# Kernel optimization log

Hardware: AMD Instinct MI355X
Metric: run time of the kernel (lower is better)

The kernel has to match this reference:

```python
import jax, jax.numpy as jnp
import numpy as np

H = 128; N = 64; B = 128; L = 3; F = 7; E = 64; LAT = 128
NEG = -1e9

def _ln(x, g, b, eps=1e-5):
    m = jnp.mean(x, axis=-1, keepdims=True)
    v = jnp.mean((x - m) ** 2, axis=-1, keepdims=True)
    return (x - m) / jnp.sqrt(v + eps) * g + b

def setup_inputs() -> dict:
    key = jax.random.key(0)
    ks = iter(jax.random.split(key, 64))
    def w(shape, s=0.05):
        return (jax.random.normal(next(ks), shape, dtype=jnp.float32) * s)
    inp = {}
    inp['battery_features'] = jax.random.normal(next(ks), (B, F), dtype=jnp.float32)
    inp['material_embeddings'] = jax.random.normal(next(ks), (B, N, E), dtype=jnp.float32)
    inp['node_mask'] = (jax.random.uniform(next(ks), (B, N)) > 0.2).astype(jnp.float32)
    # material encoder: Linear(E,H), LN, ReLU, Linear(H,H), LN, ReLU
    inp['enc_W1'] = w((E, H)); inp['enc_b1'] = jnp.zeros((H,))
    inp['enc_g1'] = jnp.ones((H,)); inp['enc_B1'] = jnp.zeros((H,))
    inp['enc_W2'] = w((H, H)); inp['enc_b2'] = jnp.zeros((H,))
    inp['enc_g2'] = jnp.ones((H,)); inp['enc_B2'] = jnp.zeros((H,))
    # per-layer GATv2 params (stacked over L layers)
    inp['Wq'] = w((L, H, H)); inp['bq'] = jnp.zeros((L, H))
    inp['Wk'] = w((L, H, H)); inp['bk'] = jnp.zeros((L, H))
    inp['Wv'] = w((L, H, H)); inp['bv'] = jnp.zeros((L, H))
    inp['We1'] = w((L, 2 * H, H)); inp['be1'] = jnp.zeros((L, H))
    inp['We2'] = w((L, H)); inp['be2'] = jnp.zeros((L,))
    inp['Wo'] = w((L, H, H)); inp['bo'] = jnp.zeros((L, H))
    inp['o_g'] = jnp.ones((L, H)); inp['o_B'] = jnp.zeros((L, H))
    # legacy decoder: Linear(F+H,H), LN, ReLU, Linear(H,LAT), LN, ReLU, Linear(LAT,F)
    inp['dW1'] = w((F + H, H)); inp['db1'] = jnp.zeros((H,))
    inp['dg1'] = jnp.ones((H,)); inp['dB1'] = jnp.zeros((H,))
    inp['dW2'] = w((H, LAT)); inp['db2'] = jnp.zeros((LAT,))
    inp['dg2'] = jnp.ones((LAT,)); inp['dB2'] = jnp.zeros((LAT,))
    inp['dW3'] = w((LAT, F)); inp['db3'] = jnp.zeros((F,))
    return inp

def reference(battery_features, material_embeddings, node_mask,
              enc_W1, enc_b1, enc_g1, enc_B1, enc_W2, enc_b2, enc_g2, enc_B2,
              Wq, bq, Wk, bk, Wv, bv, We1, be1, We2, be2, Wo, bo, o_g, o_B,
              dW1, db1, dg1, dB1, dW2, db2, dg2, dB2, dW3, db3):
    # material encoder (dropout=0 / eval)
    x = material_embeddings  # [B,N,E]
    h = jax.nn.relu(_ln(x @ enc_W1 + enc_b1, enc_g1, enc_B1))
    h = jax.nn.relu(_ln(h @ enc_W2 + enc_b2, enc_g2, enc_B2))
    x = h * node_mask[..., None]  # [B,N,H]
    mask2d = node_mask[:, :, None] * node_mask[:, None, :]  # [B,N,N]
    nlayers = Wq.shape[0]
    for l in range(nlayers):
        q = x @ Wq[l] + bq[l]
        k = x @ Wk[l] + bk[l]
        v = x @ Wv[l] + bv[l]
        # edge MLP on concat(q_i, k_j): split first linear, avoid concat materialization
        hq = q @ We1[l, :H]          # [B,N,H]
        hk = k @ We1[l, H:]          # [B,N,H]
        eh = jax.nn.relu(hq[:, :, None, :] + hk[:, None, :, :] + be1[l])  # [B,N,N,H]
        scores = jnp.einsum('bijh,h->bij', eh, We2[l]) + be2[l]
        scores = jnp.where(mask2d > 0, scores, NEG)
        attn = jax.nn.softmax(scores, axis=-1) * mask2d
        agg = jnp.einsum('bij,bjh->bih', attn, v)
        x = jax.nn.relu(_ln(agg @ Wo[l] + bo[l], o_g[l], o_B[l]))
        x = x * node_mask[..., None]
    # masked mean pooling
    denom = jnp.clip(jnp.sum(node_mask, axis=1, keepdims=True), 1.0, None)
    pooled = jnp.sum(x * node_mask[..., None], axis=1) / denom  # [B,H]
    d = jnp.concatenate([battery_features, pooled], axis=-1)
    z = jax.nn.relu(_ln(d @ dW1 + db1, dg1, dB1))
    z = jax.nn.relu(_ln(z @ dW2 + db2, dg2, dB2))
    return z @ dW3 + db3  # [B,F] predicted properties
```

## Files before the change

### kernel.cpp

```cpp
#include <hip/hip_runtime.h>


constexpr float EPS = 1e-5f;
constexpr float NEGI = -1e9f;

typedef __bf16 bf16x8 __attribute__((ext_vector_type(8)));
typedef float floatx4 __attribute__((ext_vector_type(4)));
typedef _Float16 h2 __attribute__((ext_vector_type(2)));
union U32H2 { unsigned int u; h2 h; };

__device__ __forceinline__ unsigned int pkh2(float a, float b) {
  U32H2 u; u.h[0] = (_Float16)a; u.h[1] = (_Float16)b; return u.u;
}
__device__ __forceinline__ float fdot2h(h2 a, h2 b, float c) {
#if __has_builtin(__builtin_amdgcn_fdot2)
  return __builtin_amdgcn_fdot2(a, b, c, false);
#else
  return c + (float)a[0] * (float)b[0] + (float)a[1] * (float)b[1];
#endif
}
__device__ __forceinline__ bf16x8 cvt8(const float* p) {
  float t[8];
  *(float4*)t = *(const float4*)p;
  *(float4*)(t + 4) = *(const float4*)(p + 4);
  bf16x8 r;
#pragma unroll
  for (int j = 0; j < 8; ++j) r[j] = (__bf16)t[j];
  return r;
}

__global__ __launch_bounds__(256) void prep_kernel(
    const float* __restrict__ Wq, const float* __restrict__ bq,
    const float* __restrict__ Wk, const float* __restrict__ bk,
    const float* __restrict__ bv, const float* __restrict__ We1,
    const float* __restrict__ be1,
    const float* __restrict__ eW1, const float* __restrict__ eW2,
    const float* __restrict__ Wv, const float* __restrict__ Wo,
    __bf16* __restrict__ w1pk, __bf16* __restrict__ w2pk,
    __bf16* __restrict__ wcatpk, __bf16* __restrict__ wopk,
    float* __restrict__ bcat) {
  int tid = threadIdx.x, blk = blockIdx.x;
  if (blk < 48) {
    __shared__ float sB[128 * 16];
    __shared__ float sF[128 * 17];
    int jb = blk >> 3, cc = blk & 7;
    int l = jb >> 1, w = jb & 1;
    const float* A = (w ? Wk : Wq) + l * 16384;
    const float* Bm = We1 + l * 32768 + w * 16384;
    int c0 = cc * 16;
    for (int idx = tid; idx < 2048; idx += 256) {
      int m = idx >> 4, c = idx & 15;
      sB[idx] = Bm[m * 128 + c0 + c];
    }
    __syncthreads();
    int r = tid >> 1, c8 = (tid & 1) * 8;
    float acc[8] = {};
    const float4* A4 = (const float4*)(A + r * 128);
#pragma unroll 8
    for (int k4 = 0; k4 < 32; ++k4) {
      float4 a = A4[k4];
      float av[4] = {a.x, a.y, a.z, a.w};
#pragma unroll
      for (int kk = 0; kk < 4; ++kk)
#pragma unroll
        for (int c = 0; c < 8; ++c)
          acc[c] = fmaf(av[kk], sB[(k4 * 4 + kk) * 16 + c8 + c], acc[c]);
    }
    for (int c = 0; c < 8; ++c) sF[r * 17 + c8 + c] = acc[c];
    __syncthreads();
    int kc = tid >> 6, ln = tid & 63;
    int k0 = kc * 32 + (ln >> 4) * 8, n = ln & 15;
    bf16x8 pk;
#pragma unroll
    for (int j = 0; j < 8; ++j) pk[j] = (__bf16)sF[(k0 + j) * 17 + n];
    int ntg = 8 + w * 8 + cc;
    *((bf16x8*)(wcatpk + l * 49152) + (ntg * 4 + kc) * 64 + ln) = pk;
  } else if (blk < 56) {
    int job = blk - 48;
    const float* src;
    __bf16* dst;
    int KCH = 4;
    if (job == 0) { src = eW1; dst = w1pk; KCH = 2; }
    else if (job == 1) { src = eW2; dst = w2pk; }
    else if (job < 5) { int l = job - 2; src = Wv + l * 16384; dst = wcatpk + l * 49152; }
    else { int l = job - 5; src = Wo + l * 16384; dst = wopk + l * 16384; }
    for (int s = tid; s < 8 * KCH * 64; s += 256) {
      int ln = s & 63, q = s >> 6;
      int kc = q % KCH, nt = q / KCH;
      int k0 = kc * 32 + (ln >> 4) * 8, n = nt * 16 + (ln & 15);
      bf16x8 pk;
#pragma unroll
      for (int j = 0; j < 8; ++j) pk[j] = (__bf16)src[(k0 + j) * 128 + n];
      *((bf16x8*)dst + (nt * KCH + kc) * 64 + ln) = pk;
    }
  } else {
    for (int idx = tid; idx < 3 * 384; idx += 256) {
      int l = idx / 384, c = idx % 384;
      float val;
      if (c < 128) {
        val = bv[l * 128 + c];
      } else if (c < 256) {
        int cc2 = c - 128;
        float s = 0.f;
        for (int k = 0; k < 128; ++k) s += bq[l * 128 + k] * We1[l * 32768 + k * 128 + cc2];
        val = s;
      } else {
        int cc2 = c - 256;
        float s = be1[l * 128 + cc2];
        for (int k = 0; k < 128; ++k) s += bk[l * 128 + k] * We1[l * 32768 + 16384 + k * 128 + cc2];
        val = s;
      }
      bcat[l * 384 + c] = val;
    }
  }
}

__device__ __forceinline__ void ln16(float* sT, __bf16* SX, const float* __restrict__ g,
                                     const float* __restrict__ be, float mreg,
                                     int i0, int tid, int mode) {
  int r = tid >> 4, c0 = tid & 15;
  const float* base = sT + r * 132;
  float s = 0.f, q = 0.f;
#pragma unroll
  for (int k = 0; k < 8; ++k) { float v = base[c0 + k * 16]; s += v; q += v * v; }
  s += __shfl_xor(s, 1); s += __shfl_xor(s, 2); s += __shfl_xor(s, 4); s += __shfl_xor(s, 8);
  q += __shfl_xor(q, 1); q += __shfl_xor(q, 2); q += __shfl_xor(q, 4); q += __shfl_xor(q, 8);
  float m = s * (1.f / 128.f);
  float rs = rsqrtf(fmaxf(q * (1.f / 128.f) - m * m, 0.f) + EPS);
  float mk = (mode >= 1) ? __shfl(mreg, i0 + r) : 1.f;
  int c8 = c0 * 8;
  float vals[8];
  *(float4*)vals = *(const float4*)(base + c8);
  *(float4*)(vals + 4) = *(const float4*)(base + c8 + 4);
#pragma unroll
  for (int k = 0; k < 8; ++k)
    vals[k] = fmaxf((vals[k] - m) * rs * g[c8 + k] + be[c8 + k], 0.f) * mk;
  if (mode < 2) {
    bf16x8 pk;
#pragma unroll
    for (int k = 0; k < 8; ++k) pk[k] = (__bf16)vals[k];
    ((bf16x8*)SX)[(c8 >> 5) * 64 + ((c8 >> 3) & 3) * 16 + r] = pk;
  } else {
    *(float4*)(sT + r * 132 + c8) = *(float4*)vals;
    *(float4*)(sT + r * 132 + c8 + 4) = *(float4*)(vals + 4);
  }
}

__device__ __forceinline__ void qkv_tail(
    const __bf16* SX, float* sTv, float* sTq, float* sTk,
    int b, int i0, const __bf16* __restrict__ wc, const float* __restrict__ bc,
    unsigned int* __restrict__ hqg_o, unsigned int* __restrict__ hkT_o,
    __bf16* __restrict__ vpk_o, int tid) {
  int lane = tid & 63, wv = tid >> 6, quad = lane >> 4, cl = lane & 15;
  bf16x8 ax[4];
#pragma unroll
  for (int kc = 0; kc < 4; ++kc) ax[kc] = ((const bf16x8*)SX)[kc * 64 + lane];
  floatx4 acc[6];
#pragma unroll
  for (int n = 0; n < 6; ++n) acc[n] = 0;
#pragma unroll
  for (int kc = 0; kc < 4; ++kc)
#pragma unroll
    for (int n = 0; n < 6; ++n) {
      bf16x8 bw = ((const bf16x8*)wc)[((wv + n * 4) * 4 + kc) * 64 + lane];
      acc[n] = __builtin_amdgcn_mfma_f32_16x16x32_bf16(ax[kc], bw, acc[n], 0, 0, 0);
    }
#pragma unroll
  for (int n = 0; n < 6; ++n) {
    int nt = wv + n * 4;
    float* dstT;
    int coll;
    float bb;
    if (nt < 8) { dstT = sTv; coll = nt * 16 + cl; bb = bc[coll]; }
    else if (nt < 16) { dstT = sTq; coll = (nt - 8) * 16 + cl; bb = bc[128 + coll]; }
    else { dstT = sTk; coll = (nt - 16) * 16 + cl; bb = bc[256 + coll]; }
#pragma unroll
    for (int r = 0; r < 4; ++r) dstT[(quad * 4 + r) * 132 + coll] = acc[n][r] + bb;
  }
  __syncthreads();
  {
    int nt = tid >> 5, dq = (tid >> 4) & 1, c2 = tid & 15;
    int kcv = i0 >> 5, qg = ((i0 & 31) >> 3) + dq;
    bf16x8 pk;
#pragma unroll
    for (int jj = 0; jj < 8; ++jj) pk[jj] = (__bf16)sTv[(dq * 8 + jj) * 132 + nt * 16 + c2];
    ((bf16x8*)vpk_o)[b * 1024 + (nt * 2 + kcv) * 64 + qg * 16 + c2] = pk;
  }
  {
    int r = tid >> 4, c0 = tid & 15;
    float vq[8];
    *(float4*)vq = *(const float4*)(sTq + r * 132 + c0 * 8);
    *(float4*)(vq + 4) = *(const float4*)(sTq + r * 132 + c0 * 8 + 4);
    uint4 oq;
    oq.x = pkh2(vq[0], vq[1]); oq.y = pkh2(vq[2], vq[3]);
    oq.z = pkh2(vq[4], vq[5]); oq.w = pkh2(vq[6], vq[7]);
    *(uint4*)(hqg_o + (b * 64 + i0 + r) * 64 + c0 * 4) = oq;
  }
  {
    int jr = tid & 15, hpg = tid >> 4;
    float vk[8];
    *(float4*)vk = *(const float4*)(sTk + jr * 132 + hpg * 8);
    *(float4*)(vk + 4) = *(const float4*)(sTk + jr * 132 + hpg * 8 + 4);
    int jg = i0 + jr;
#pragma unroll
    for (int t = 0; t < 4; ++t)
      hkT_o[b * 4096 + (hpg * 4 + t) * 64 + jg] = pkh2(vk[2 * t], vk[2 * t + 1]);
  }
}

__global__ __launch_bounds__(256) void enc_qkv_kernel(
    const float* __restrict__ emb, const float* __restrict__ mask,
    const float* __restrict__ eb1, const float* __restrict__ eg1, const float* __restrict__ eB1,
    const float* __restrict__ eb2, const float* __restrict__ eg2, const float* __restrict__ eB2,
    const __bf16* __restrict__ w1pk, const __bf16* __restrict__ w2pk,
    const __bf16* __restrict__ wcat0, const float* __restrict__ bcat0,
    unsigned int* __restrict__ hqg, unsigned int* __restrict__ hkT,
    __bf16* __restrict__ vpk) {
  __shared__ __align__(16) float sT[16 * 132];
  __shared__ __align__(16) __bf16 SX[2048];
  __shared__ __align__(16) float sTv[16 * 132], sTq[16 * 132], sTk[16 * 132];
  int tid = threadIdx.x, blk = blockIdx.x;
  int lane = tid & 63, wv = tid >> 6, quad = lane >> 4, cl = lane & 15;
  int b = blk >> 2, i0 = (blk & 3) * 16;
  float mreg = mask[b * 64 + lane];

  {
    bf16x8 a1[2];
#pragma unroll
    for (int kc = 0; kc < 2; ++kc)
      a1[kc] = cvt8(emb + (b * 64 + i0 + cl) * 64 + kc * 32 + quad * 8);
    floatx4 acc[2];
    acc[0] = 0; acc[1] = 0;
#pragma unroll
    for (int kc = 0; kc < 2; ++kc)
#pragma unroll
      for (int n = 0; n < 2; ++n) {
        bf16x8 bw = ((const bf16x8*)w1pk)[((wv + n * 4) * 2 + kc) * 64 + lane];
        acc[n] = __builtin_amdgcn_mfma_f32_16x16x32_bf16(a1[kc], bw, acc[n], 0, 0, 0);
      }
#pragma unroll
    for (int n = 0; n < 2; ++n) {
      int col = (wv + n * 4) * 16 + cl;
      float bb = eb1[col];
#pragma unroll
      for (int r = 0; r < 4; ++r) sT[(quad * 4 + r) * 132 + col] = acc[n][r] + bb;
    }
  }
  __syncthreads();
  ln16(sT, SX, eg1, eB1, mreg, i0, tid, 0);
  __syncthreads();
  {
    bf16x8 a2[4];
#pragma unroll
    for (int kc = 0; kc < 4; ++kc) a2[kc] = ((const bf16x8*)SX)[kc * 64 + lane];
    floatx4 acc[2];
    acc[0] = 0; acc[1] = 0;
#pragma unroll
    for (int kc = 0; kc < 4; ++kc)
#pragma unroll
      for (int n = 0; n < 2; ++n) {
        bf16x8 bw = ((const bf16x8*)w2pk)[((wv + n * 4) * 4 + kc) * 64 + lane];
        acc[n] = __builtin_amdgcn_mfma_f32_16x16x32_bf16(a2[kc], bw, acc[n], 0, 0, 0);
      }
#pragma unroll
    for (int n = 0; n < 2; ++n) {
      int col = (wv + n * 4) * 16 + cl;
      float bb = eb2[col];
#pragma unroll
      for (int r = 0; r < 4; ++r) sT[(quad * 4 + r) * 132 + col] = acc[n][r] + bb;
    }
  }
  __syncthreads();
  ln16(sT, SX, eg2, eB2, mreg, i0, tid, 1);
  __syncthreads();
  qkv_tail(SX, sTv, sTq, sTk, b, i0, wcat0, bcat0, hqg, hkT, vpk, tid);
}

template <bool LAST>
__global__ __launch_bounds__(256) void layer_kernel(
    const unsigned int* __restrict__ hq_in, const unsigned int* __restrict__ hkT_in,
    const __bf16* __restrict__ vp_in, const float* __restrict__ mask,
    const float* __restrict__ We2l, const float* __restrict__ be2p,
    const __bf16* __restrict__ wopk_l, const float* __restrict__ bo_l,
    const float* __restrict__ og_l, const float* __restrict__ oB_l,
    const __bf16* __restrict__ wcat_n, const float* __restrict__ bcat_n,
    unsigned int* __restrict__ hq_out, unsigned int* __restrict__ hkT_out,
    __bf16* __restrict__ vpk_out, float* __restrict__ poolp) {
  __shared__ __align__(16) unsigned int sHK[64 * 64];
  __shared__ __align__(16) unsigned int hqS[16 * 64];
  __shared__ unsigned int w2h[64];
  __shared__ __align__(16) __bf16 pA[16 * 64];
  __shared__ __align__(16) __bf16 pA2[2048];
  __shared__ __align__(16) __bf16 SX[2048];
  __shared__ __align__(16) float sT[16 * 132];
  __shared__ __align__(16) float sTv[16 * 132], sTq[16 * 132], sTk[16 * 132];
  int tid = threadIdx.x, blk = blockIdx.x;
  int lane = tid & 63, wv = tid >> 6, quad = lane >> 4, cl = lane & 15;
  int b = blk >> 2, i0 = (blk & 3) * 16;
  float mreg = mask[b * 64 + lane];

  {
    const uint4* src = (const uint4*)(hkT_in + b * 4096);
    uint4* dst = (uint4*)sHK;
#pragma unroll
    for (int it = 0; it < 4; ++it) dst[it * 256 + tid] = src[it * 256 + tid];
    ((uint4*)hqS)[tid] = ((const uint4*)(hq_in + (b * 64 + i0) * 64))[tid];
    if (tid < 64) w2h[tid] = pkh2(We2l[2 * tid], We2l[2 * tid + 1]);
  }
  __syncthreads();

  {
    int j = lane;
    float accs[4] = {0.f, 0.f, 0.f, 0.f};
    h2 hz = {(_Float16)0.0f, (_Float16)0.0f};
#pragma unroll 4
    for (int c4 = 0; c4 < 16; ++c4) {
      uint4 w2v = *(const uint4*)(w2h + c4 * 4);
      int hp0 = c4 * 4;
      uint4 hkv;
      hkv.x = sHK[(hp0 + 0) * 64 + j];
      hkv.y = sHK[(hp0 + 1) * 64 + j];
      hkv.z = sHK[(hp0 + 2) * 64 + j];
      hkv.w = sHK[(hp0 + 3) * 64 + j];
#pragma unroll
      for (int il = 0; il < 4; ++il) {
        uint4 hqv = *(const uint4*)(hqS + (wv * 4 + il) * 64 + hp0);
        U32H2 ha, hb, wc2;
        h2 s2;
        ha.u = hqv.x; hb.u = hkv.x; wc2.u = w2v.x;
        s2 = __builtin_elementwise_max(ha.h + hb.h, hz);
        accs[il] = fdot2h(s2, wc2.h, accs[il]);
        ha.u = hqv.y; hb.u = hkv.y; wc2.u = w2v.y;
        s2 = __builtin_elementwise_max(ha.h + hb.h, hz);
        accs[il] = fdot2h(s2, wc2.h, accs[il]);
        ha.u = hqv.z; hb.u = hkv.z; wc2.u = w2v.z;
        s2 = __builtin_elementwise_max(ha.h + hb.h, hz);
        accs[il] = fdot2h(s2, wc2.h, accs[il]);
        ha.u = hqv.w; hb.u = hkv.w; wc2.u = w2v.w;
        s2 = __builtin_elementwise_max(ha.h + hb.h, hz);
        accs[il] = fdot2h(s2, wc2.h, accs[il]);
      }
    }
    float be2v = be2p[0];
    float mj = mreg;
#pragma unroll
    for (int kk = 0; kk < 4; ++kk) {
      int il = wv * 4 + kk;
      float mi = __shfl(mreg, i0 + il);
      float m2 = mi * mj;
      float sc = (m2 > 0.f) ? accs[kk] + be2v : NEGI;
      float mx = sc;
#pragma unroll
      for (int off = 32; off >= 1; off >>= 1) mx = fmaxf(mx, __shfl_xor(mx, off));
      float p = __expf(sc - mx);
      float sm = p;
#pragma unroll
      for (int off = 32; off >= 1; off >>= 1) sm += __shfl_xor(sm, off);
      float a = p / sm * m2;
      pA[((j >> 5) * 64 + ((j >> 3) & 3) * 16 + il) * 8 + (j & 7)] = (__bf16)a;
    }
  }
  __syncthreads();

  {
    bf16x8 aat[2];
#pragma unroll
    for (int kc = 0; kc < 2; ++kc) aat[kc] = ((const bf16x8*)pA)[kc * 64 + lane];
    floatx4 acc[2];
    acc[0] = 0; acc[1] = 0;
#pragma unroll
    for (int kc = 0; kc < 2; ++kc)
#pragma unroll
      for (int n = 0; n < 2; ++n) {
        bf16x8 bw = ((const bf16x8*)vp_in)[b * 1024 + ((wv + n * 4) * 2 + kc) * 64 + lane];
        acc[n] = __builtin_amdgcn_mfma_f32_16x16x32_bf16(aat[kc], bw, acc[n], 0, 0, 0);
      }
#pragma unroll
    for (int n = 0; n < 2; ++n) {
      int hcol = (wv + n * 4) * 16 + cl;
#pragma unroll
      for (int r = 0; r < 4; ++r) {
        int i = quad * 4 + r;
        pA2[((hcol >> 5) * 64 + ((hcol >> 3) & 3) * 16 + i) * 8 + (hcol & 7)] =
            (__bf16)acc[n][r];
      }
    }
  }
  __syncthreads();

  {
    bf16x8 ag[4];
#pragma unroll
    for (int kc = 0; kc < 4; ++kc) ag[kc] = ((const bf16x8*)pA2)[kc * 64 + lane];
    floatx4 acc[2];
    acc[0] = 0; acc[1] = 0;
#pragma unroll
    for (int kc = 0; kc < 4; ++kc)
#pragma unroll
      for (int n = 0; n < 2; ++n) {
        bf16x8 bw = ((const bf16x8*)wopk_l)[((wv + n * 4) * 4 + kc) * 64 + lane];
        acc[n] = __builtin_amdgcn_mfma_f32_16x16x32_bf16(ag[kc], bw, acc[n], 0, 0, 0);
      }
#pragma unroll
    for (int n = 0; n < 2; ++n) {
      int col = (wv + n * 4) * 16 + cl;
      float bb = bo_l[col];
#pragma unroll
      for (int r = 0; r < 4; ++r) sT[(quad * 4 + r) * 132 + col] = acc[n][r] + bb;
    }
  }
  __syncthreads();
  ln16(sT, SX, og_l, oB_l, mreg, i0, tid, LAST ? 2 : 1);
  __syncthreads();
  if (!LAST) {
    qkv_tail(SX, sTv, sTq, sTk, b, i0, wcat_n, bcat_n, hq_out, hkT_out, vpk_out, tid);
  } else {
    if (tid < 128) {
      float s = 0.f;
#pragma unroll
      for (int r = 0; r < 16; ++r) s += sT[r * 132 + tid];
      poolp[blk * 128 + tid] = s;
    }
  }
}

__device__ __forceinline__ float ln128(float val, float g, float be, int t, float* red) {
  float s = val, q = val * val;
#pragma unroll
  for (int off = 32; off >= 1; off >>= 1) {
    s += __shfl_xor(s, off);
    q += __shfl_xor(q, off);
  }
  if ((t & 63) == 0) { red[(t >> 6) * 2] = s; red[(t >> 6) * 2 + 1] = q; }
  __syncthreads();
  float S = red[0] + red[2], Q = red[1] + red[3];
  __syncthreads();
  float m = S * (1.f / 128.f);
  float var = Q * (1.f / 128.f) - m * m;
  float r = rsqrtf(fmaxf(var, 0.f) + EPS);
  return (val - m) * r * g + be;
}

__global__ __launch_bounds__(128) void dec_kernel(
    const float* __restrict__ bfeat, const float* __restrict__ poolp,
    const float* __restrict__ mask,
    const float* __restrict__ dW1, const float* __restrict__ db1,
    const float* __restrict__ dg1, const float* __restrict__ dB1,
    const float* __restrict__ dW2, const float* __restrict__ db2,
    const float* __restrict__ dg2, const float* __restrict__ dB2,
    const float* __restrict__ dW3, const float* __restrict__ db3,
    float* __restrict__ out) {
  __shared__ float sd[136];
  __shared__ float sz[128];
  __shared__ float red[4];
  __shared__ float s_mk[64];
  int b = blockIdx.x, t = threadIdx.x;
  if (t < 64) s_mk[t] = mask[b * 64 + t];
  __syncthreads();
  float den = 0.f;
#pragma unroll
  for (int i = 0; i < 64; ++i) den += s_mk[i];
  den = fmaxf(den, 1.f);
  float pooled = poolp[(b * 4 + 0) * 128 + t] + poolp[(b * 4 + 1) * 128 + t] +
                 poolp[(b * 4 + 2) * 128 + t] + poolp[(b * 4 + 3) * 128 + t];
  if (t < 7) sd[t] = bfeat[b * 7 + t];
  sd[7 + t] = pooled / den;
  __syncthreads();

  float z = db1[t];
  for (int k = 0; k < 135; ++k) z = fmaf(sd[k], dW1[k * 128 + t], z);
  z = ln128(z, dg1[t], dB1[t], t, red);
  z = fmaxf(z, 0.f);
  sz[t] = z;
  __syncthreads();

  float z2 = db2[t];
  for (int k = 0; k < 128; ++k) z2 = fmaf(sz[k], dW2[k * 128 + t], z2);
  z2 = ln128(z2, dg2[t], dB2[t], t, red);
  z2 = fmaxf(z2, 0.f);
  sz[t] = z2;
  __syncthreads();

  if (t < 7) {
    float o = db3[t];
    for (int k = 0; k < 128; ++k) o = fmaf(sz[k], dW3[k * 7 + t], o);
    out[b * 7 + t] = o;
  }
}

extern "C" void kernel_launch(void* const* d_in, const int* in_sizes, int n_in,
                              void* d_out, int out_size, void* d_ws, size_t ws_size,
                              hipStream_t stream) {
  const float* bf   = (const float*)d_in[0];
  const float* emb  = (const float*)d_in[1];
  const float* mask = (const float*)d_in[2];
  const float* eW1 = (const float*)d_in[3];
  const float* eb1 = (const float*)d_in[4];
  const float* eg1 = (const float*)d_in[5];
  const float* eB1 = (const float*)d_in[6];
  const float* eW2 = (const float*)d_in[7];
  const float* eb2 = (const float*)d_in[8];
  const float* eg2 = (const float*)d_in[9];
  const float* eB2 = (const float*)d_in[10];
  const float* Wq = (const float*)d_in[11];
  const float* bq = (const float*)d_in[12];
  const float* Wk = (const float*)d_in[13];
  const float* bk = (const float*)d_in[14];
  const float* Wv = (const float*)d_in[15];
  const float* bv = (const float*)d_in[16];
  const float* We1 = (const float*)d_in[17];
  const float* be1 = (const float*)d_in[18];
  const float* We2 = (const float*)d_in[19];
  const float* be2 = (const float*)d_in[20];
  const float* Wo = (const float*)d_in[21];
  const float* bo = (const float*)d_in[22];
  const float* og = (const float*)d_in[23];
  const float* oB = (const float*)d_in[24];
  const float* dW1 = (const float*)d_in[25];
  const float* db1 = (const float*)d_in[26];
  const float* dg1 = (const float*)d_in[27];
  const float* dB1 = (const float*)d_in[28];
  const float* dW2 = (const float*)d_in[29];
  const float* db2 = (const float*)d_in[30];
  const float* dg2 = (const float*)d_in[31];
  const float* dB2 = (const float*)d_in[32];
  const float* dW3 = (const float*)d_in[33];
  const float* db3 = (const float*)d_in[34];
  float* out = (float*)d_out;

  char* ws = (char*)d_ws;
  float* bcat = (float*)ws;
  __bf16* w1pk   = (__bf16*)(ws + 8192);
  __bf16* w2pk   = (__bf16*)(ws + 24576);
  __bf16* wcatpk = (__bf16*)(ws + 57344);
  __bf16* wopk   = (__bf16*)(ws + 352256);
  unsigned int* hqg = (unsigned int*)(ws + 524288);
  unsigned int* hkT = (unsigned int*)(ws + 4718592);
  __bf16* vpk = (__bf16*)(ws + 8912896);
  float* poolp = (float*)(ws + 13107200);

  prep_kernel<<<57, 256, 0, stream>>>(Wq, bq, Wk, bk, bv, We1, be1,
                                      eW1, eW2, Wv, Wo, w1pk, w2pk, wcatpk, wopk, bcat);
  enc_qkv_kernel<<<512, 256, 0, stream>>>(emb, mask, eb1, eg1, eB1, eb2, eg2, eB2,
                                          w1pk, w2pk, wcatpk, bcat, hqg, hkT, vpk);
  layer_kernel<false><<<512, 256, 0, stream>>>(
      hqg, hkT, vpk, mask, We2, be2, wopk, bo, og, oB,
      wcatpk + 49152, bcat + 384,
      hqg + 524288, hkT + 524288, vpk + 1048576, nullptr);
  layer_kernel<false><<<512, 256, 0, stream>>>(
      hqg + 524288, hkT + 524288, vpk + 1048576, mask, We2 + 128, be2 + 1,
      wopk + 16384, bo + 128, og + 128, oB + 128,
      wcatpk + 2 * 49152, bcat + 2 * 384,
      hqg, hkT, vpk, nullptr);
  layer_kernel<true><<<512, 256, 0, stream>>>(
      hqg, hkT, vpk, mask, We2 + 256, be2 + 2,
      wopk + 2 * 16384, bo + 256, og + 256, oB + 256,
      nullptr, nullptr, nullptr, nullptr, nullptr, poolp);
  dec_kernel<<<128, 128, 0, stream>>>(bf, poolp, mask, dW1, db1, dg1, dB1,
                                      dW2, db2, dg2, dB2, dW3, db3, out);
}
```

Measured before the change: 204.5 us.

## Fuse decoder into last layer via atomic counter, cut LDS for occupancy

The separate decoder kernel is removed. The last block of each batch, found with an atomic per-batch counter, runs the decoder MLP inside the final layer kernel, so one launch and its gap go away. The key tensor is now read straight from global memory instead of being staged in LDS. Shared buffers are aliased into one byte array and launch bounds request 4 blocks per SM, to raise occupancy. The cost is uncached global reads in the score loop, an added memset, and cross-block synchronization through atomics.

```diff
diff --git a/kernel.cpp b/kernel.cpp
--- a/kernel.cpp
+++ b/kernel.cpp
@@ -216,9 +216,9 @@
     const __bf16* __restrict__ wcat0, const float* __restrict__ bcat0,
     unsigned int* __restrict__ hqg, unsigned int* __restrict__ hkT,
     __bf16* __restrict__ vpk) {
-  __shared__ __align__(16) float sT[16 * 132];
   __shared__ __align__(16) __bf16 SX[2048];
   __shared__ __align__(16) float sTv[16 * 132], sTq[16 * 132], sTk[16 * 132];
+  float* sT = sTv;
   int tid = threadIdx.x, blk = blockIdx.x;
   int lane = tid & 63, wv = tid >> 6, quad = lane >> 4, cl = lane & 15;
   int b = blk >> 2, i0 = (blk & 3) * 16;
@@ -277,7 +277,7 @@
 }
 
 template <bool LAST>
-__global__ __launch_bounds__(256) void layer_kernel(
+__global__ __launch_bounds__(256, 4) void layer_kernel(
     const unsigned int* __restrict__ hq_in, const unsigned int* __restrict__ hkT_in,
     const __bf16* __restrict__ vp_in, const float* __restrict__ mask,
     const float* __restrict__ We2l, const float* __restrict__ be2p,
@@ -285,25 +285,31 @@
     const float* __restrict__ og_l, const float* __restrict__ oB_l,
     const __bf16* __restrict__ wcat_n, const float* __restrict__ bcat_n,
     unsigned int* __restrict__ hq_out, unsigned int* __restrict__ hkT_out,
-    __bf16* __restrict__ vpk_out, float* __restrict__ poolp) {
-  __shared__ __align__(16) unsigned int sHK[64 * 64];
-  __shared__ __align__(16) unsigned int hqS[16 * 64];
-  __shared__ unsigned int w2h[64];
-  __shared__ __align__(16) __bf16 pA[16 * 64];
-  __shared__ __align__(16) __bf16 pA2[2048];
-  __shared__ __align__(16) __bf16 SX[2048];
-  __shared__ __align__(16) float sT[16 * 132];
-  __shared__ __align__(16) float sTv[16 * 132], sTq[16 * 132], sTk[16 * 132];
+    __bf16* __restrict__ vpk_out, float* __restrict__ poolp,
+    unsigned int* __restrict__ bctr, const float* __restrict__ bfeat,
+    const float* __restrict__ dW1, const float* __restrict__ db1,
+    const float* __restrict__ dg1, const float* __restrict__ dB1,
+    const float* __restrict__ dW2, const float* __restrict__ db2,
+    const float* __restrict__ dg2, const float* __restrict__ dB2,
+    const float* __restrict__ dW3, const float* __restrict__ db3,
+    float* __restrict__ out) {
+  __shared__ __align__(16) char SM[40960];
+  unsigned int* hqS = (unsigned int*)(SM + 0);
+  unsigned int* w2h = (unsigned int*)(SM + 4096);
+  __bf16* pA  = (__bf16*)(SM + 4352);
+  __bf16* pA2 = (__bf16*)(SM + 6400);
+  __bf16* SX  = (__bf16*)(SM + 10496);
+  float* sT   = (float*)(SM + 14592);
+  float* sTv  = sT;
+  float* sTq  = (float*)(SM + 23040);
+  float* sTk  = (float*)(SM + 31488);
+  unsigned int* flg = (unsigned int*)(SM + 39936);
   int tid = threadIdx.x, blk = blockIdx.x;
   int lane = tid & 63, wv = tid >> 6, quad = lane >> 4, cl = lane & 15;
   int b = blk >> 2, i0 = (blk & 3) * 16;
   float mreg = mask[b * 64 + lane];
 
   {
-    const uint4* src = (const uint4*)(hkT_in + b * 4096);
-    uint4* dst = (uint4*)sHK;
-#pragma unroll
-    for (int it = 0; it < 4; ++it) dst[it * 256 + tid] = src[it * 256 + tid];
     ((uint4*)hqS)[tid] = ((const uint4*)(hq_in + (b * 64 + i0) * 64))[tid];
     if (tid < 64) w2h[tid] = pkh2(We2l[2 * tid], We2l[2 * tid + 1]);
   }
@@ -311,6 +317,7 @@
 
   {
     int j = lane;
+    const unsigned int* hkg = hkT_in + b * 4096;
     float accs[4] = {0.f, 0.f, 0.f, 0.f};
     h2 hz = {(_Float16)0.0f, (_Float16)0.0f};
 #pragma unroll 4
@@ -318,10 +325,10 @@
       uint4 w2v = *(const uint4*)(w2h + c4 * 4);
       int hp0 = c4 * 4;
       uint4 hkv;
-      hkv.x = sHK[(hp0 + 0) * 64 + j];
-      hkv.y = sHK[(hp0 + 1) * 64 + j];
-      hkv.z = sHK[(hp0 + 2) * 64 + j];
-      hkv.w = sHK[(hp0 + 3) * 64 + j];
+      hkv.x = hkg[(hp0 + 0) * 64 + j];
+      hkv.y = hkg[(hp0 + 1) * 64 + j];
+      hkv.z = hkg[(hp0 + 2) * 64 + j];
+      hkv.w = hkg[(hp0 + 3) * 64 + j];
 #pragma unroll
       for (int il = 0; il < 4; ++il) {
         uint4 hqv = *(const uint4*)(hqS + (wv * 4 + il) * 64 + hp0);
@@ -421,70 +428,80 @@
       for (int r = 0; r < 16; ++r) s += sT[r * 132 + tid];
       poolp[blk * 128 + tid] = s;
     }
-  }
-}
-
-__device__ __forceinline__ float ln128(float val, float g, float be, int t, float* red) {
-  float s = val, q = val * val;
-#pragma unroll
-  for (int off = 32; off >= 1; off >>= 1) {
-    s += __shfl_xor(s, off);
-    q += __shfl_xor(q, off);
-  }
-  if ((t & 63) == 0) { red[(t >> 6) * 2] = s; red[(t >> 6) * 2 + 1] = q; }
-  __syncthreads();
-  float S = red[0] + red[2], Q = red[1] + red[3];
-  __syncthreads();
-  float m = S * (1.f / 128.f);
-  float var = Q * (1.f / 128.f) - m * m;
-  float r = rsqrtf(fmaxf(var, 0.f) + EPS);
-  return (val - m) * r * g + be;
-}
-
-__global__ __launch_bounds__(128) void dec_kernel(
-    const float* __restrict__ bfeat, const float* __restrict__ poolp,
-    const float* __restrict__ mask,
-    const float* __restrict__ dW1, const float* __restrict__ db1,
-    const float* __restrict__ dg1, const float* __restrict__ dB1,
-    const float* __restrict__ dW2, const float* __restrict__ db2,
-    const float* __restrict__ dg2, const float* __restrict__ dB2,
-    const float* __restrict__ dW3, const float* __restrict__ db3,
-    float* __restrict__ out) {
-  __shared__ float sd[136];
-  __shared__ float sz[128];
-  __shared__ float red[4];
-  __shared__ float s_mk[64];
-  int b = blockIdx.x, t = threadIdx.x;
-  if (t < 64) s_mk[t] = mask[b * 64 + t];
-  __syncthreads();
-  float den = 0.f;
-#pragma unroll
-  for (int i = 0; i < 64; ++i) den += s_mk[i];
-  den = fmaxf(den, 1.f);
-  float pooled = poolp[(b * 4 + 0) * 128 + t] + poolp[(b * 4 + 1) * 128 + t] +
-                 poolp[(b * 4 + 2) * 128 + t] + poolp[(b * 4 + 3) * 128 + t];
-  if (t < 7) sd[t] = bfeat[b * 7 + t];
-  sd[7 + t] = pooled / den;
-  __syncthreads();
-
-  float z = db1[t];
-  for (int k = 0; k < 135; ++k) z = fmaf(sd[k], dW1[k * 128 + t], z);
-  z = ln128(z, dg1[t], dB1[t], t, red);
-  z = fmaxf(z, 0.f);
-  sz[t] = z;
-  __syncthreads();
-
-  float z2 = db2[t];
-  for (int k = 0; k < 128; ++k) z2 = fmaf(sz[k], dW2[k * 128 + t], z2);
-  z2 = ln128(z2, dg2[t], dB2[t], t, red);
-  z2 = fmaxf(z2, 0.f);
-  sz[t] = z2;
-  __syncthreads();
-
-  if (t < 7) {
-    float o = db3[t];
-    for (int k = 0; k < 128; ++k) o = fmaf(sz[k], dW3[k * 7 + t], o);
-    out[b * 7 + t] = o;
+    __syncthreads();
+    if (tid == 0) {
+      __threadfence();
+      unsigned int old = __hip_atomic_fetch_add(bctr + b, 1u, __ATOMIC_ACQ_REL,
+                                                __HIP_MEMORY_SCOPE_AGENT);
+      *flg = old;
+    }
+    __syncthreads();
+    if (*flg != 3u) return;
+    __threadfence();
+
+    float* sd   = (float*)(SM + 0);
+    float* red  = (float*)(SM + 4096);
+    float* part = (float*)(SM + 6400);
+    float* szz  = (float*)(SM + 10496);
+    float den = mreg;
+#pragma unroll
+    for (int off = 32; off >= 1; off >>= 1) den += __shfl_xor(den, off);
+    den = fmaxf(den, 1.f);
+    if (tid < 7) sd[tid] = bfeat[b * 7 + tid];
+    if (tid < 128) {
+      float pooled = poolp[(b * 4 + 0) * 128 + tid] + poolp[(b * 4 + 1) * 128 + tid] +
+                     poolp[(b * 4 + 2) * 128 + tid] + poolp[(b * 4 + 3) * 128 + tid];
+      sd[7 + tid] = pooled / den;
+    }
+    __syncthreads();
+    int t = tid & 127, g2 = tid >> 7;
+    {
+      float zp = 0.f;
+      for (int k = g2; k < 135; k += 2) zp = fmaf(sd[k], dW1[k * 128 + t], zp);
+      part[g2 * 128 + t] = zp;
+    }
+    __syncthreads();
+    {
+      float z = db1[t] + part[t] + part[128 + t];
+      float s = z, q = z * z;
+#pragma unroll
+      for (int off = 32; off >= 1; off >>= 1) { s += __shfl_xor(s, off); q += __shfl_xor(q, off); }
+      if (tid < 128 && lane == 0) { red[(tid >> 6) * 2] = s; red[(tid >> 6) * 2 + 1] = q; }
+      __syncthreads();
+      float S = red[0] + red[2], Q = red[1] + red[3];
+      float m = S * (1.f / 128.f);
+      float rs = rsqrtf(fmaxf(Q * (1.f / 128.f) - m * m, 0.f) + EPS);
+      z = fmaxf((z - m) * rs * dg1[t] + dB1[t], 0.f);
+      __syncthreads();
+      if (tid < 128) szz[t] = z;
+    }
+    __syncthreads();
+    {
+      float zp = 0.f;
+      for (int k = g2; k < 128; k += 2) zp = fmaf(szz[k], dW2[k * 128 + t], zp);
+      part[g2 * 128 + t] = zp;
+    }
+    __syncthreads();
+    {
+      float y = db2[t] + part[t] + part[128 + t];
+      float s = y, q = y * y;
+#pragma unroll
+      for (int off = 32; off >= 1; off >>= 1) { s += __shfl_xor(s, off); q += __shfl_xor(q, off); }
+      if (tid < 128 && lane == 0) { red[(tid >> 6) * 2] = s; red[(tid >> 6) * 2 + 1] = q; }
+      __syncthreads();
+      float S = red[0] + red[2], Q = red[1] + red[3];
+      float m = S * (1.f / 128.f);
+      float rs = rsqrtf(fmaxf(Q * (1.f / 128.f) - m * m, 0.f) + EPS);
+      y = fmaxf((y - m) * rs * dg2[t] + dB2[t], 0.f);
+      __syncthreads();
+      if (tid < 128) szz[t] = y;
+    }
+    __syncthreads();
+    if (tid < 7) {
+      float o = db3[tid];
+      for (int k = 0; k < 128; ++k) o = fmaf(szz[k], dW3[k * 7 + tid], o);
+      out[b * 7 + tid] = o;
+    }
   }
 }
 
@@ -529,7 +546,8 @@
   float* out = (float*)d_out;
 
   char* ws = (char*)d_ws;
-  float* bcat = (float*)ws;
+  unsigned int* bctr = (unsigned int*)ws;
+  float* bcat = (float*)(ws + 1024);
   __bf16* w1pk   = (__bf16*)(ws + 8192);
   __bf16* w2pk   = (__bf16*)(ws + 24576);
   __bf16* wcatpk = (__bf16*)(ws + 57344);
@@ -539,6 +557,8 @@
   __bf16* vpk = (__bf16*)(ws + 8912896);
   float* poolp = (float*)(ws + 13107200);
 
+  hipMemsetAsync(d_ws, 0, 512, stream);
+
   prep_kernel<<<57, 256, 0, stream>>>(Wq, bq, Wk, bk, bv, We1, be1,
                                       eW1, eW2, Wv, Wo, w1pk, w2pk, wcatpk, wopk, bcat);
   enc_qkv_kernel<<<512, 256, 0, stream>>>(emb, mask, eb1, eg1, eB1, eb2, eg2, eB2,
@@ -546,16 +566,19 @@
   layer_kernel<false><<<512, 256, 0, stream>>>(
       hqg, hkT, vpk, mask, We2, be2, wopk, bo, og, oB,
       wcatpk + 49152, bcat + 384,
-      hqg + 524288, hkT + 524288, vpk + 1048576, nullptr);
+      hqg + 524288, hkT + 524288, vpk + 1048576, nullptr,
+      nullptr, nullptr, nullptr, nullptr, nullptr, nullptr,
+      nullptr, nullptr, nullptr, nullptr, nullptr, nullptr, nullptr);
   layer_kernel<false><<<512, 256, 0, stream>>>(
       hqg + 524288, hkT + 524288, vpk + 1048576, mask, We2 + 128, be2 + 1,
       wopk + 16384, bo + 128, og + 128, oB + 128,
       wcatpk + 2 * 49152, bcat + 2 * 384,
-      hqg, hkT, vpk, nullptr);
+      hqg, hkT, vpk, nullptr,
+      nullptr, nullptr, nullptr, nullptr, nullptr, nullptr,
+      nullptr, nullptr, nullptr, nullptr, nullptr, nullptr, nullptr);
   layer_kernel<true><<<512, 256, 0, stream>>>(
       hqg, hkT, vpk, mask, We2 + 256, be2 + 2,
       wopk + 2 * 16384, bo + 256, og + 256, oB + 256,
-      nullptr, nullptr, nullptr, nullptr, nullptr, poolp);
-  dec_kernel<<<128, 128, 0, stream>>>(bf, poolp, mask, dW1, db1, dg1, dB1,
-                                      dW2, db2, dg2, dB2, dW3, db3, out);
-}
+      nullptr, nullptr, nullptr, nullptr, nullptr, poolp,
+      bctr, bf, dW1, db1, dg1, dB1, dW2, db2, dg2, dB2, dW3, db3, out);
+}
```

New measurement: 254.6 us. 24.5% more time.

## Cut LDS footprint in layer kernel to raise occupancy, read hk from global

Applied to the files above, without the earlier changes.

The layer kernel no longer stages the per-batch transposed hk tile (16 KB) in LDS. Each wave now loads it directly from global memory, relying on L1/L2 to serve the four blocks that share a batch. The remaining shared buffers are packed into one 40 KB array with sT aliased onto sTv, and launch_bounds now asks for 4 blocks per CU. The encoder kernel also aliases sT onto sTv. The trade is higher occupancy against global-memory latency in the hot score loop. The bcat workspace offset also moves.

```diff
diff --git a/kernel.cpp b/kernel.cpp
--- a/kernel.cpp
+++ b/kernel.cpp
@@ -216,9 +216,9 @@
     const __bf16* __restrict__ wcat0, const float* __restrict__ bcat0,
     unsigned int* __restrict__ hqg, unsigned int* __restrict__ hkT,
     __bf16* __restrict__ vpk) {
-  __shared__ __align__(16) float sT[16 * 132];
   __shared__ __align__(16) __bf16 SX[2048];
   __shared__ __align__(16) float sTv[16 * 132], sTq[16 * 132], sTk[16 * 132];
+  float* sT = sTv;
   int tid = threadIdx.x, blk = blockIdx.x;
   int lane = tid & 63, wv = tid >> 6, quad = lane >> 4, cl = lane & 15;
   int b = blk >> 2, i0 = (blk & 3) * 16;
@@ -277,7 +277,7 @@
 }
 
 template <bool LAST>
-__global__ __launch_bounds__(256) void layer_kernel(
+__global__ __launch_bounds__(256, 4) void layer_kernel(
     const unsigned int* __restrict__ hq_in, const unsigned int* __restrict__ hkT_in,
     const __bf16* __restrict__ vp_in, const float* __restrict__ mask,
     const float* __restrict__ We2l, const float* __restrict__ be2p,
@@ -286,24 +286,22 @@
     const __bf16* __restrict__ wcat_n, const float* __restrict__ bcat_n,
     unsigned int* __restrict__ hq_out, unsigned int* __restrict__ hkT_out,
     __bf16* __restrict__ vpk_out, float* __restrict__ poolp) {
-  __shared__ __align__(16) unsigned int sHK[64 * 64];
-  __shared__ __align__(16) unsigned int hqS[16 * 64];
-  __shared__ unsigned int w2h[64];
-  __shared__ __align__(16) __bf16 pA[16 * 64];
-  __shared__ __align__(16) __bf16 pA2[2048];
-  __shared__ __align__(16) __bf16 SX[2048];
-  __shared__ __align__(16) float sT[16 * 132];
-  __shared__ __align__(16) float sTv[16 * 132], sTq[16 * 132], sTk[16 * 132];
+  __shared__ __align__(16) char SM[40960];
+  unsigned int* hqS = (unsigned int*)(SM + 0);
+  unsigned int* w2h = (unsigned int*)(SM + 4096);
+  __bf16* pA  = (__bf16*)(SM + 4352);
+  __bf16* pA2 = (__bf16*)(SM + 6400);
+  __bf16* SX  = (__bf16*)(SM + 10496);
+  float* sT   = (float*)(SM + 14592);
+  float* sTv  = sT;
+  float* sTq  = (float*)(SM + 23040);
+  float* sTk  = (float*)(SM + 31488);
   int tid = threadIdx.x, blk = blockIdx.x;
   int lane = tid & 63, wv = tid >> 6, quad = lane >> 4, cl = lane & 15;
   int b = blk >> 2, i0 = (blk & 3) * 16;
   float mreg = mask[b * 64 + lane];
 
   {
-    const uint4* src = (const uint4*)(hkT_in + b * 4096);
-    uint4* dst = (uint4*)sHK;
-#pragma unroll
-    for (int it = 0; it < 4; ++it) dst[it * 256 + tid] = src[it * 256 + tid];
     ((uint4*)hqS)[tid] = ((const uint4*)(hq_in + (b * 64 + i0) * 64))[tid];
     if (tid < 64) w2h[tid] = pkh2(We2l[2 * tid], We2l[2 * tid + 1]);
   }
@@ -311,6 +309,7 @@
 
   {
     int j = lane;
+    const unsigned int* hkg = hkT_in + b * 4096;
     float accs[4] = {0.f, 0.f, 0.f, 0.f};
     h2 hz = {(_Float16)0.0f, (_Float16)0.0f};
 #pragma unroll 4
@@ -318,10 +317,10 @@
       uint4 w2v = *(const uint4*)(w2h + c4 * 4);
       int hp0 = c4 * 4;
       uint4 hkv;
-      hkv.x = sHK[(hp0 + 0) * 64 + j];
-      hkv.y = sHK[(hp0 + 1) * 64 + j];
-      hkv.z = sHK[(hp0 + 2) * 64 + j];
-      hkv.w = sHK[(hp0 + 3) * 64 + j];
+      hkv.x = hkg[(hp0 + 0) * 64 + j];
+      hkv.y = hkg[(hp0 + 1) * 64 + j];
+      hkv.z = hkg[(hp0 + 2) * 64 + j];
+      hkv.w = hkg[(hp0 + 3) * 64 + j];
 #pragma unroll
       for (int il = 0; il < 4; ++il) {
         uint4 hqv = *(const uint4*)(hqS + (wv * 4 + il) * 64 + hp0);
@@ -529,7 +528,7 @@
   float* out = (float*)d_out;
 
   char* ws = (char*)d_ws;
-  float* bcat = (float*)ws;
+  float* bcat = (float*)(ws + 1024);
   __bf16* w1pk   = (__bf16*)(ws + 8192);
   __bf16* w2pk   = (__bf16*)(ws + 24576);
   __bf16* wcatpk = (__bf16*)(ws + 57344);
```

New measurement: 201.6 us. About the same (-1.4%).
